# Optimization experiments

Measured on AMD Instinct MI355X. Metric: run time of the kernel, lower is better.

## Reference

```python
import jax, jax.numpy as jnp
import numpy as np

N_EMBED = 384
N_HEAD = 6
HEAD_DIM = N_EMBED // N_HEAD


def setup_inputs() -> dict:
    key = jax.random.key(0)
    k1, k2, k3 = jax.random.split(key, 3)
    B, T = 128, 256
    x = jax.random.normal(k1, (B, T, N_EMBED), dtype=jnp.float32)
    # nn.Linear(N_EMBED, 3*N_EMBED, bias=False): weight [3*N_EMBED, N_EMBED],
    # applied as x @ W.T -> store transposed [N_EMBED, 3*N_EMBED]
    W_qkv = jax.random.normal(k2, (N_EMBED, 3 * N_EMBED), dtype=jnp.float32) * (N_EMBED ** -0.5)
    W_proj = jax.random.normal(k3, (N_EMBED, N_EMBED), dtype=jnp.float32) * (N_EMBED ** -0.5)
    return {"x": x, "W_qkv": W_qkv, "W_proj": W_proj}


def reference(x, W_qkv, W_proj):
    B, T, C = x.shape
    qkv = jnp.einsum('btc,cd->btd', x, W_qkv)  # [B,T,3C]
    q, k, v = jnp.split(qkv, 3, axis=-1)
    # [B, H, T, Dh]
    q = q.reshape(B, T, N_HEAD, HEAD_DIM).transpose(0, 2, 1, 3)
    k = k.reshape(B, T, N_HEAD, HEAD_DIM).transpose(0, 2, 1, 3)
    v = v.reshape(B, T, N_HEAD, HEAD_DIM).transpose(0, 2, 1, 3)
    scale = HEAD_DIM ** -0.5
    wei = jnp.einsum('bhqd,bhkd->bhqk', q, k) * scale  # [B,H,T,T]
    causal = jnp.tril(jnp.ones((T, T), dtype=bool))
    wei = jnp.where(causal[None, None, :, :], wei, -jnp.inf)
    wei = jax.nn.softmax(wei, axis=-1)
    # dropout layers are identity in eval mode
    out = jnp.einsum('bhqk,bhkd->bhqd', wei, v)  # [B,H,T,Dh]
    out = out.transpose(0, 2, 1, 3).reshape(B, T, C)
    out = jnp.einsum('btc,cd->btd', out, W_proj)
    return out
```

## Files before the change

kernel.cpp:

```cpp
#include <hip/hip_runtime.h>
#include <hip/hip_bf16.h>

typedef __attribute__((ext_vector_type(8))) short short8;
typedef __attribute__((ext_vector_type(4))) float f32x4;
typedef __attribute__((ext_vector_type(4))) unsigned short ush4;

typedef const __attribute__((address_space(1))) void* gas_p;
typedef __attribute__((address_space(3))) void* las_p;
#define GLOAD_LDS16(g, l) __builtin_amdgcn_global_load_lds((gas_p)(const void*)(g), (las_p)(void*)(l), 16, 0, 0)

__device__ __forceinline__ unsigned short f2bf(float f) {
    union { float f; unsigned int u; } v; v.f = f;
    unsigned int r = v.u + 0x7FFFu + ((v.u >> 16) & 1u);
    return (unsigned short)(r >> 16);
}
__device__ __forceinline__ unsigned pk2(float a, float b) {
    return (unsigned)f2bf(a) | ((unsigned)f2bf(b) << 16);
}

__global__ __launch_bounds__(256) void cast_all_kernel(
    const float* __restrict__ x, const float* __restrict__ Wqkv, const float* __restrict__ Wproj,
    unsigned short* __restrict__ xb, unsigned short* __restrict__ wqkvt,
    unsigned short* __restrict__ wprojt)
{
    const int bid = blockIdx.x;
    if (bid < 6144) {
        int i = bid * 256 + threadIdx.x;
        const float4* p = (const float4*)x + (size_t)i * 2;
        float4 a = p[0], b = p[1];
        short8 o;
        o[0] = (short)f2bf(a.x); o[1] = (short)f2bf(a.y);
        o[2] = (short)f2bf(a.z); o[3] = (short)f2bf(a.w);
        o[4] = (short)f2bf(b.x); o[5] = (short)f2bf(b.y);
        o[6] = (short)f2bf(b.z); o[7] = (short)f2bf(b.w);
        *(short8*)(xb + (size_t)i * 8) = o;
    } else if (bid < 7872) {
        int idx = (bid - 6144) * 256 + threadIdx.x;
        int n = idx / 384, k = idx - n * 384;
        wqkvt[idx] = f2bf(Wqkv[(size_t)k * 1152 + n]);
    } else {
        int idx = (bid - 7872) * 256 + threadIdx.x;
        int n = idx / 384, k = idx - n * 384;
        wprojt[idx] = f2bf(Wproj[(size_t)k * 384 + n]);
    }
}

template<int MODE, int NP>
__global__ __launch_bounds__(256, 2) void gemm_bt_kernel(
    const unsigned short* __restrict__ A, const unsigned short* __restrict__ Bt,
    void* __restrict__ C0, unsigned short* __restrict__ C1,
    int M, int N, int K)
{
    __shared__ __align__(16) unsigned short As[128 * 64];
    __shared__ __align__(16) unsigned short Bs[128 * 64];
    const int tid = threadIdx.x;
    const int lane = tid & 63, wv = tid >> 6;
    const int c = lane & 15, g = lane >> 4;
    const int wm = (wv >> 1) * 64, wn = (wv & 1) * 64;

    const int mpx = (M >> 7) >> 3;
    const int id = blockIdx.x, xcd = id & 7, kk = id >> 3;
    const long m0 = (long)(xcd * mpx + kk / NP) * 128;
    const long n0 = (long)(kk % NP) * 128;

    f32x4 acc[4][4] = {};
    const int xr = (c & 7) << 4;

    for (int kt = 0; kt < K; kt += 64) {
        #pragma unroll
        for (int i = 0; i < 4; ++i) {
            int ch = i * 256 + wv * 64 + lane;
            int row = ch >> 3, cc = ch & 7;
            int sc = (cc ^ (row & 7)) * 8;
            GLOAD_LDS16(&A[(m0 + row) * (size_t)K + kt + sc],
                        &As[(i * 256 + wv * 64) * 8]);
            GLOAD_LDS16(&Bt[(n0 + row) * (size_t)K + kt + sc],
                        &Bs[(i * 256 + wv * 64) * 8]);
        }
        __syncthreads();
        #pragma unroll
        for (int ks = 0; ks < 2; ++ks) {
            short8 af[4], bf_[4];
            #pragma unroll
            for (int i = 0; i < 4; ++i)
                af[i] = *(const short8*)((char*)As +
                    (((wm + i * 16 + c) * 128 + (ks * 32 + g * 8) * 2) ^ xr));
            #pragma unroll
            for (int i = 0; i < 4; ++i)
                bf_[i] = *(const short8*)((char*)Bs +
                    (((wn + i * 16 + c) * 128 + (ks * 32 + g * 8) * 2) ^ xr));
            #pragma unroll
            for (int mi = 0; mi < 4; ++mi)
                #pragma unroll
                for (int ni = 0; ni < 4; ++ni)
                    acc[mi][ni] = __builtin_amdgcn_mfma_f32_16x16x32_bf16(
                        af[mi], bf_[ni], acc[mi][ni], 0, 0, 0);
        }
        __syncthreads();
    }

    if (MODE == 1) {
        #pragma unroll
        for (int mi = 0; mi < 4; ++mi)
            #pragma unroll
            for (int ni = 0; ni < 4; ++ni)
                #pragma unroll
                for (int r = 0; r < 4; ++r) {
                    long m = m0 + wm + mi * 16 + g * 4 + r;
                    long n = n0 + wn + ni * 16 + c;
                    ((float*)C0)[m * N + n] = acc[mi][ni][r];
                }
    } else if (n0 < 768) {
        #pragma unroll
        for (int mi = 0; mi < 4; ++mi)
            #pragma unroll
            for (int ni = 0; ni < 4; ++ni)
                #pragma unroll
                for (int r = 0; r < 4; ++r) {
                    long m = m0 + wm + mi * 16 + g * 4 + r;
                    long n = n0 + wn + ni * 16 + c;
                    ((unsigned short*)C0)[m * 768 + n] = f2bf(acc[mi][ni][r]);
                }
    } else {
        char* wbase = (char*)As + wv * 8192;
        #pragma unroll
        for (int ni = 0; ni < 4; ++ni)
            #pragma unroll
            for (int mi = 0; mi < 4; ++mi)
                #pragma unroll
                for (int r = 0; r < 4; ++r) {
                    int d = ni * 16 + c, t = mi * 16 + g * 4 + r;
                    int byte = (d * 128 + t * 2) ^ ((d & 7) << 4);
                    *(unsigned short*)(wbase + byte) = f2bf(acc[mi][ni][r]);
                }
        __asm__ __volatile__("" ::: "memory");
        int h = (int)((n0 + wn - 768) >> 6);
        long b = (m0 + wm) >> 8;
        int t0 = (int)((m0 + wm) & 255);
        long bh = b * 6 + h;
        #pragma unroll
        for (int it = 0; it < 8; ++it) {
            int d = it * 8 + (lane >> 3), ck = lane & 7;
            short8 v = *(const short8*)(wbase + ((d * 128 + ck * 16) ^ ((d & 7) << 4)));
            *(short8*)&C1[(bh * 64 + d) * 256 + t0 + ck * 8] = v;
        }
    }
}

__global__ __launch_bounds__(256, 3) void attn_kernel(
    const unsigned short* __restrict__ qk,
    const unsigned short* __restrict__ vt,
    unsigned short* __restrict__ outp)
{
    const int bh = blockIdx.x;
    const int b = bh / 6, h = bh - b * 6;
    const int tid = threadIdx.x;
    const int lane = tid & 63, wv = tid >> 6;
    const int c = lane & 15, g = lane >> 4;

    __shared__ unsigned short Ks[256 * 64];
    __shared__ unsigned short Pl[4][16 * 64];

    #pragma unroll
    for (int it = 0; it < 8; ++it) {
        int ch = it * 256 + tid;
        int row = ch >> 3, col = (ch & 7) * 8;
        int db = (row * 128 + col * 2) ^ ((row & 7) << 4);
        *(short8*)((char*)Ks + db) =
            *(const short8*)&qk[(size_t)(b * 256 + row) * 768 + 384 + h * 64 + col];
    }
    __syncthreads();

    char* plw = (char*)Pl[wv];

    for (int t = 0; t < 2; ++t) {
        const int p = t ? 7 - wv : wv;
        const int jlast = p >> 1;
        const int modd = (p & 1) * 32;
        const int qt0 = p * 32;

        short8 aq[2][2];
        #pragma unroll
        for (int mi = 0; mi < 2; ++mi)
            #pragma unroll
            for (int ks = 0; ks < 2; ++ks)
                aq[mi][ks] = *(const short8*)&qk[
                    (size_t)(b * 256 + qt0 + mi * 16 + c) * 768 + h * 64 + ks * 32 + g * 8];

        f32x4 o[2][4] = {};
        float mrun[2] = {-1e30f, -1e30f}, lrun[2] = {0.f, 0.f};

        for (int j = 0; j <= jlast; ++j) {
            short8 bv[4][2];
            #pragma unroll
            for (int nd = 0; nd < 4; ++nd)
                #pragma unroll
                for (int ks = 0; ks < 2; ++ks)
                    bv[nd][ks] = *(const short8*)&vt[
                        ((size_t)bh * 64 + nd * 16 + c) * 256 + j * 64 + ks * 32 + g * 8];

            short8 bk[4][2];
            #pragma unroll
            for (int ni = 0; ni < 4; ++ni)
                #pragma unroll
                for (int ks = 0; ks < 2; ++ks) {
                    int key = j * 64 + ni * 16 + c;
                    bk[ni][ks] = *(const short8*)((char*)Ks +
                        ((key * 128 + (ks * 32 + g * 8) * 2) ^ ((key & 7) << 4)));
                }

            #pragma unroll
            for (int mi = 0; mi < 2; ++mi) {
                float pv[4][4];
                #pragma unroll
                for (int ni = 0; ni < 4; ++ni) {
                    f32x4 z = {0.f, 0.f, 0.f, 0.f};
                    z = __builtin_amdgcn_mfma_f32_16x16x32_bf16(bk[ni][0], aq[mi][0], z, 0, 0, 0);
                    z = __builtin_amdgcn_mfma_f32_16x16x32_bf16(bk[ni][1], aq[mi][1], z, 0, 0, 0);
                    #pragma unroll
                    for (int r = 0; r < 4; ++r) {
                        float v = z[r] * 0.125f;
                        if (j == jlast) {
                            int kloc = ni * 16 + g * 4 + r;
                            int qloc = mi * 16 + c + modd;
                            if (kloc > qloc) v = -1e30f;
                        }
                        pv[ni][r] = v;
                    }
                }
                float m01 = fmaxf(fmaxf(pv[0][0], pv[0][1]), fmaxf(pv[0][2], pv[0][3]));
                float m11 = fmaxf(fmaxf(pv[1][0], pv[1][1]), fmaxf(pv[1][2], pv[1][3]));
                float m21 = fmaxf(fmaxf(pv[2][0], pv[2][1]), fmaxf(pv[2][2], pv[2][3]));
                float m31 = fmaxf(fmaxf(pv[3][0], pv[3][1]), fmaxf(pv[3][2], pv[3][3]));
                float m1 = fmaxf(fmaxf(m01, m11), fmaxf(m21, m31));
                m1 = fmaxf(m1, __shfl_xor(m1, 16));
                m1 = fmaxf(m1, __shfl_xor(m1, 32));
                float mold = mrun[mi];
                float mnew = fmaxf(mold, m1);
                float fac = __expf(mold - mnew);
                float ssum = 0.f;
                #pragma unroll
                for (int ni = 0; ni < 4; ++ni)
                    #pragma unroll
                    for (int r = 0; r < 4; ++r) {
                        float pp = __expf(pv[ni][r] - mnew);
                        pv[ni][r] = pp;
                        ssum += pp;
                    }
                ssum += __shfl_xor(ssum, 16);
                ssum += __shfl_xor(ssum, 32);
                lrun[mi] = lrun[mi] * fac + ssum;
                mrun[mi] = mnew;
                #pragma unroll
                for (int nd = 0; nd < 4; ++nd)
                    #pragma unroll
                    for (int r = 0; r < 4; ++r) o[mi][nd][r] *= fac;

                __asm__ __volatile__("" ::: "memory");
                #pragma unroll
                for (int ni = 0; ni < 4; ++ni) {
                    uint2 w;
                    w.x = pk2(pv[ni][0], pv[ni][1]);
                    w.y = pk2(pv[ni][2], pv[ni][3]);
                    *(uint2*)(plw + ((c * 128 + ni * 32 + g * 8) ^ ((c & 7) << 4))) = w;
                }
                __asm__ __volatile__("" ::: "memory");

                short8 ap[2];
                #pragma unroll
                for (int ks = 0; ks < 2; ++ks)
                    ap[ks] = *(const short8*)(plw +
                        ((c * 128 + ks * 64 + g * 16) ^ ((c & 7) << 4)));

                #pragma unroll
                for (int nd = 0; nd < 4; ++nd) {
                    o[mi][nd] = __builtin_amdgcn_mfma_f32_16x16x32_bf16(bv[nd][0], ap[0], o[mi][nd], 0, 0, 0);
                    o[mi][nd] = __builtin_amdgcn_mfma_f32_16x16x32_bf16(bv[nd][1], ap[1], o[mi][nd], 0, 0, 0);
                }
                __asm__ __volatile__("" ::: "memory");
            }
        }

        #pragma unroll
        for (int mi = 0; mi < 2; ++mi) {
            float inv = 1.0f / lrun[mi];
            #pragma unroll
            for (int nd = 0; nd < 4; ++nd) {
                ush4 w;
                #pragma unroll
                for (int r = 0; r < 4; ++r) w[r] = f2bf(o[mi][nd][r] * inv);
                *(ush4*)&outp[((size_t)b * 256 + qt0 + mi * 16 + c) * 384 + h * 64 + nd * 16 + g * 4] = w;
            }
        }
    }
}

extern "C" void kernel_launch(void* const* d_in, const int* in_sizes, int n_in,
                              void* d_out, int out_size, void* d_ws, size_t ws_size,
                              hipStream_t stream) {
    const float* x     = (const float*)d_in[0];
    const float* Wqkv  = (const float*)d_in[1];
    const float* Wproj = (const float*)d_in[2];

    char* ws = (char*)d_ws;
    unsigned short* xb     = (unsigned short*)(ws);
    unsigned short* wqkvt  = (unsigned short*)(ws + 25165824);
    unsigned short* wprojt = (unsigned short*)(ws + 26050560);
    unsigned short* qkb    = (unsigned short*)(ws + 26345472);
    unsigned short* vtb    = (unsigned short*)(ws + 76677120);
    unsigned short* attnb  = (unsigned short*)(ws + 101842944);

    cast_all_kernel<<<8448, 256, 0, stream>>>(x, Wqkv, Wproj, xb, wqkvt, wprojt);

    gemm_bt_kernel<0, 9><<<2304, 256, 0, stream>>>(xb, wqkvt, (void*)qkb, vtb, 32768, 1152, 384);
    attn_kernel<<<768, 256, 0, stream>>>(qkb, vtb, attnb);
    gemm_bt_kernel<1, 3><<<768, 256, 0, stream>>>(attnb, wprojt, d_out, nullptr, 32768, 384, 384);
}
```

Measured before the change: 106.6 us.

## Double-buffer B tile in GEMM and prefetch next B during compute

Grows shared memory to three 128x64 tiles so the B operand is double-buffered and the next B tile load is issued before the MFMA loop on the current one. A stays single-buffered and is reloaded after compute behind an extra barrier. The intent is to hide part of the global-to-LDS load latency. In exchange it adds a second sync per iteration, leaves the A load exposed, and uses more LDS per block.

New measurement: 105.2 us, median of 3. No clear change (-1.3%).

```diff
diff --git a/kernel.cpp b/kernel.cpp
--- a/kernel.cpp
+++ b/kernel.cpp
@@ -51,8 +51,8 @@
     void* __restrict__ C0, unsigned short* __restrict__ C1,
     int M, int N, int K)
 {
-    __shared__ __align__(16) unsigned short As[128 * 64];
-    __shared__ __align__(16) unsigned short Bs[128 * 64];
+    __shared__ __align__(16) unsigned short Sh[3 * 128 * 64];
+    unsigned short* As = Sh;
     const int tid = threadIdx.x;
     const int lane = tid & 63, wv = tid >> 6;
     const int c = lane & 15, g = lane >> 4;
@@ -66,18 +66,38 @@
     f32x4 acc[4][4] = {};
     const int xr = (c & 7) << 4;
 
-    for (int kt = 0; kt < K; kt += 64) {
-        #pragma unroll
-        for (int i = 0; i < 4; ++i) {
-            int ch = i * 256 + wv * 64 + lane;
-            int row = ch >> 3, cc = ch & 7;
-            int sc = (cc ^ (row & 7)) * 8;
-            GLOAD_LDS16(&A[(m0 + row) * (size_t)K + kt + sc],
-                        &As[(i * 256 + wv * 64) * 8]);
-            GLOAD_LDS16(&Bt[(n0 + row) * (size_t)K + kt + sc],
-                        &Bs[(i * 256 + wv * 64) * 8]);
-        }
-        __syncthreads();
+    int chrow[4], chsc[4];
+    #pragma unroll
+    for (int i = 0; i < 4; ++i) {
+        int ch = i * 256 + wv * 64 + lane;
+        chrow[i] = ch >> 3;
+        chsc[i] = ((ch & 7) ^ (chrow[i] & 7)) * 8;
+    }
+
+#define STAGE_A(kt)                                                            \
+    {                                                                          \
+        _Pragma("unroll")                                                      \
+        for (int i = 0; i < 4; ++i)                                            \
+            GLOAD_LDS16(&A[(m0 + chrow[i]) * (size_t)K + (kt) + chsc[i]],      \
+                        &As[(i * 256 + wv * 64) * 8]);                         \
+    }
+#define STAGE_B(bufofs, kt)                                                    \
+    {                                                                          \
+        _Pragma("unroll")                                                      \
+        for (int i = 0; i < 4; ++i)                                            \
+            GLOAD_LDS16(&Bt[(n0 + chrow[i]) * (size_t)K + (kt) + chsc[i]],     \
+                        &Sh[(bufofs) + (i * 256 + wv * 64) * 8]);              \
+    }
+
+    STAGE_A(0);
+    STAGE_B(8192, 0);
+    __syncthreads();
+
+    const int nt = K >> 6;
+    for (int t = 0; t < nt; ++t) {
+        const int bofs = 8192 + (t & 1) * 8192;
+        if (t + 1 < nt) STAGE_B(8192 + ((t + 1) & 1) * 8192, (t + 1) * 64);
+        const unsigned short* Bcur = Sh + bofs;
         #pragma unroll
         for (int ks = 0; ks < 2; ++ks) {
             short8 af[4], bf_[4];
@@ -87,7 +107,7 @@
                     (((wm + i * 16 + c) * 128 + (ks * 32 + g * 8) * 2) ^ xr));
             #pragma unroll
             for (int i = 0; i < 4; ++i)
-                bf_[i] = *(const short8*)((char*)Bs +
+                bf_[i] = *(const short8*)((char*)Bcur +
                     (((wn + i * 16 + c) * 128 + (ks * 32 + g * 8) * 2) ^ xr));
             #pragma unroll
             for (int mi = 0; mi < 4; ++mi)
@@ -97,7 +117,13 @@
                         af[mi], bf_[ni], acc[mi][ni], 0, 0, 0);
         }
         __syncthreads();
-    }
+        if (t + 1 < nt) {
+            STAGE_A((t + 1) * 64);
+            __syncthreads();
+        }
+    }
+#undef STAGE_A
+#undef STAGE_B
 
     if (MODE == 1) {
         #pragma unroll
@@ -122,7 +148,7 @@
                     ((unsigned short*)C0)[m * 768 + n] = f2bf(acc[mi][ni][r]);
                 }
     } else {
-        char* wbase = (char*)As + wv * 8192;
+        char* wbase = (char*)Sh + wv * 8192;
         #pragma unroll
         for (int ni = 0; ni < 4; ++ni)
             #pragma unroll
```
